# Kernel tuning notes

Hardware: AMD Instinct MI355X
Metric: run time of the kernel (lower is better)

## Reference

```python
import jax, jax.numpy as jnp
import numpy as np

EMBED_DIM = 384
HEADS = 6
HEAD_DIM = EMBED_DIM // HEADS
WINDOW = 64


def setup_inputs() -> dict:
    key = jax.random.key(0)
    ks = jax.random.split(key, 5)
    B, T = 128, 256
    s_attn = 1.0 / np.sqrt(EMBED_DIM)
    x = jax.random.normal(ks[0], (B, T, EMBED_DIM), dtype=jnp.float32)
    W_attn = jax.random.normal(ks[1], (EMBED_DIM, 3 * EMBED_DIM), dtype=jnp.float32) * s_attn
    b_attn = jax.random.normal(ks[2], (3 * EMBED_DIM,), dtype=jnp.float32) * 0.02
    W_proj = jax.random.normal(ks[3], (EMBED_DIM, EMBED_DIM), dtype=jnp.float32) * s_attn
    b_proj = jax.random.normal(ks[4], (EMBED_DIM,), dtype=jnp.float32) * 0.02
    return {"x": x, "W_attn": W_attn, "b_attn": b_attn, "W_proj": W_proj, "b_proj": b_proj}


def reference(x, W_attn, b_attn, W_proj, b_proj):
    B, T, C = x.shape
    qkv = x @ W_attn + b_attn  # [B,T,3C]
    q, k, v = jnp.split(qkv, 3, axis=-1)
    # [B, H, T, hd]
    q = q.reshape(B, T, HEADS, HEAD_DIM).transpose(0, 2, 1, 3)
    k = k.reshape(B, T, HEADS, HEAD_DIM).transpose(0, 2, 1, 3)
    v = v.reshape(B, T, HEADS, HEAD_DIM).transpose(0, 2, 1, 3)
    scale = 1.0 / np.sqrt(HEAD_DIM).astype(np.float32)
    att = jnp.einsum('bhqd,bhkd->bhqk', q, k) * scale
    i = jnp.arange(T)
    causal = i[:, None] >= i[None, :]
    local = jnp.abs(i[:, None] - i[None, :]) <= WINDOW
    mask = (causal & local)[None, None, :, :]
    att = jnp.where(mask, att, -jnp.inf)
    att = jax.nn.softmax(att, axis=-1)
    y = jnp.einsum('bhqk,bhkd->bhqd', att, v)
    y = y.transpose(0, 2, 1, 3).reshape(B, T, C)
    return y @ W_proj + b_proj
```

## Files before the change

kernel.cpp:

```cpp
#include <hip/hip_runtime.h>

#define B_SZ   128
#define T_SEQ  256
#define C_DIM  384
#define HEADS  6
#define HD     64
#define WIN    64

typedef __bf16 bf16x8 __attribute__((ext_vector_type(8)));
typedef float  f32x4  __attribute__((ext_vector_type(4)));

typedef __attribute__((address_space(3))) void lds_void;
typedef __attribute__((address_space(1))) void gbl_void;

__device__ __forceinline__ unsigned short f2bf(float f) {
  unsigned u = __float_as_uint(f);
  u += 0x7FFFu + ((u >> 16) & 1u);
  return (unsigned short)(u >> 16);
}

__global__ __launch_bounds__(256) void convert_f32_bf16(
    const float* __restrict__ in, unsigned short* __restrict__ out, int n4) {
  int i = blockIdx.x * blockDim.x + threadIdx.x;
  if (i < n4) {
    float4 v = ((const float4*)in)[i];
    ushort4 o;
    o.x = f2bf(v.x); o.y = f2bf(v.y); o.z = f2bf(v.z); o.w = f2bf(v.w);
    ((ushort4*)out)[i] = o;
  }
}

__global__ __launch_bounds__(256) void transpose_convert(
    const float* __restrict__ in, unsigned short* __restrict__ out,
    int K, int N) {
  __shared__ float tile[32][33];
  const int gx = blockIdx.x * 32;
  const int gy = blockIdx.y * 32;
  const int tx = threadIdx.x;
  const int ty = threadIdx.y;
#pragma unroll
  for (int r = ty; r < 32; r += 8)
    tile[r][tx] = in[(size_t)(gy + r) * N + gx + tx];
  __syncthreads();
#pragma unroll
  for (int r = ty; r < 32; r += 8)
    out[(size_t)(gx + r) * K + gy + tx] = f2bf(tile[tx][r]);
}

template <bool OUT_BF16>
__global__ __launch_bounds__(256) void gemm_mfma_bf16(
    const unsigned short* __restrict__ A,
    const unsigned short* __restrict__ Bt,
    const float* __restrict__ bias,
    void* __restrict__ Cv, int M, int N, int K) {
  __shared__ unsigned short As[128 * 64];
  __shared__ unsigned short Bs[128 * 64];

  const int t    = threadIdx.x;
  const int lane = t & 63;
  const int w    = t >> 6;
  const int wm   = w & 1;
  const int wn   = w >> 1;
  const int m0   = blockIdx.y * 128;
  const int n0   = blockIdx.x * 128;

  const int lrow = lane >> 3;
  const int lcol = lane & 7;
  const int schunk = lcol ^ lrow;

  f32x4 acc[4][4];
#pragma unroll
  for (int i = 0; i < 4; ++i)
#pragma unroll
    for (int j = 0; j < 4; ++j) acc[i][j] = (f32x4){0.f, 0.f, 0.f, 0.f};

  const int mfrag = lane & 15;
  const int quad  = lane >> 4;
  const int sw    = mfrag & 7;

  for (int k0 = 0; k0 < K; k0 += 64) {
#pragma unroll
    for (int i = 0; i < 4; ++i) {
      const int inst = w * 4 + i;
      const int r = inst * 8 + lrow;
      const unsigned short* ga = A  + (size_t)(m0 + r) * K + k0 + schunk * 8;
      const unsigned short* gb = Bt + (size_t)(n0 + r) * K + k0 + schunk * 8;
      __builtin_amdgcn_global_load_lds((const gbl_void*)ga,
                                       (lds_void*)(As + inst * 512), 16, 0, 0);
      __builtin_amdgcn_global_load_lds((const gbl_void*)gb,
                                       (lds_void*)(Bs + inst * 512), 16, 0, 0);
    }
    __syncthreads();

#pragma unroll
    for (int ks = 0; ks < 64; ks += 32) {
      const int cg = (ks >> 3) + quad;
      const int cp = (cg ^ sw) << 3;
      bf16x8 af[4], bfr[4];
#pragma unroll
      for (int mt = 0; mt < 4; ++mt)
        af[mt] = *(const bf16x8*)(As + (size_t)(wm * 64 + mt * 16 + mfrag) * 64 + cp);
#pragma unroll
      for (int nt = 0; nt < 4; ++nt)
        bfr[nt] = *(const bf16x8*)(Bs + (size_t)(wn * 64 + nt * 16 + mfrag) * 64 + cp);
#pragma unroll
      for (int mt = 0; mt < 4; ++mt)
#pragma unroll
        for (int nt = 0; nt < 4; ++nt)
          acc[mt][nt] = __builtin_amdgcn_mfma_f32_16x16x32_bf16(
              af[mt], bfr[nt], acc[mt][nt], 0, 0, 0);
    }
    __syncthreads();
  }

  const int ccol = lane & 15;
  const int crow = (lane >> 4) * 4;
#pragma unroll
  for (int nt = 0; nt < 4; ++nt) {
    const int col = n0 + wn * 64 + nt * 16 + ccol;
    const float bv = bias[col];
#pragma unroll
    for (int mt = 0; mt < 4; ++mt) {
#pragma unroll
      for (int r = 0; r < 4; ++r) {
        const int row = m0 + wm * 64 + mt * 16 + crow + r;
        const float val = acc[mt][nt][r] + bv;
        if (OUT_BF16)
          ((unsigned short*)Cv)[(size_t)row * N + col] = f2bf(val);
        else
          ((float*)Cv)[(size_t)row * N + col] = val;
      }
    }
  }
}

#define PSTR 68
__global__ __launch_bounds__(256) void attn_mfma(
    const unsigned short* __restrict__ qkv, unsigned short* __restrict__ y) {
  __shared__ unsigned short Qs[64 * 64];
  __shared__ unsigned short Ks[64 * 64];
  __shared__ unsigned short Vt[64 * 64];
  __shared__ float Pw[4][16 * PSTR];

  const int bid = blockIdx.x;
  const int qt  = bid & 3;
  const int h   = (bid >> 2) % HEADS;
  const int b   = bid / (4 * HEADS);
  const int t   = threadIdx.x;
  const int lane = t & 63;
  const int w    = t >> 6;
  const int quad = lane >> 4;
  const int m16  = lane & 15;
  const int sw   = m16 & 7;

  const size_t rowbase = (size_t)b * T_SEQ * (3 * C_DIM);
  const int qoff = h * HD;
  const int koff = C_DIM + h * HD;
  const int voff = 2 * C_DIM + h * HD;
  const int qg0  = qt * 64;

  const int lrow = lane >> 3;
  const int lcol = lane & 7;
  const int schunk = lcol ^ lrow;

#pragma unroll
  for (int i = 0; i < 2; ++i) {
    const int inst = w * 2 + i;
    const int r = inst * 8 + lrow;
    const unsigned short* ga =
        qkv + rowbase + (size_t)(qg0 + r) * (3 * C_DIM) + qoff + schunk * 8;
    __builtin_amdgcn_global_load_lds((const gbl_void*)ga,
                                     (lds_void*)(Qs + inst * 512), 16, 0, 0);
  }

  float m_r[4], l_r[4];
  f32x4 yacc[4];
#pragma unroll
  for (int r = 0; r < 4; ++r) { m_r[r] = -1e30f; l_r[r] = 0.f; }
#pragma unroll
  for (int dt = 0; dt < 4; ++dt) yacc[dt] = (f32x4){0.f, 0.f, 0.f, 0.f};

  const int nchunks  = (qt == 0) ? 1 : 2;
  const int kb_first = (qt == 0) ? 0 : (qg0 - 64);
  const int qrow_base = qg0 + w * 16 + quad * 4;

  for (int ch = 0; ch < nchunks; ++ch) {
    const int kb = kb_first + ch * 64;

    __syncthreads();

#pragma unroll
    for (int i = 0; i < 2; ++i) {
      const int inst = w * 2 + i;
      const int r = inst * 8 + lrow;
      const unsigned short* ga =
          qkv + rowbase + (size_t)(kb + r) * (3 * C_DIM) + koff + schunk * 8;
      __builtin_amdgcn_global_load_lds((const gbl_void*)ga,
                                       (lds_void*)(Ks + inst * 512), 16, 0, 0);
    }
    {
      const int vkey = t & 63;
      const int kc = vkey >> 3, ke = vkey & 7;
      const int vd0  = (t >> 6) * 16;
      const unsigned short* gv =
          qkv + rowbase + (size_t)(kb + vkey) * (3 * C_DIM) + voff + vd0;
#pragma unroll
      for (int u = 0; u < 4; ++u) {
        ushort4 vv = *(const ushort4*)(gv + u * 4);
#pragma unroll
        for (int jj = 0; jj < 4; ++jj) {
          const int d = vd0 + u * 4 + jj;
          const unsigned short val =
              (jj == 0) ? vv.x : (jj == 1) ? vv.y : (jj == 2) ? vv.z : vv.w;
          Vt[d * 64 + ((kc ^ (d & 7)) << 3) + ke] = val;
        }
      }
    }
    __syncthreads();

    f32x4 sacc[4];
#pragma unroll
    for (int nt = 0; nt < 4; ++nt) sacc[nt] = (f32x4){0.f, 0.f, 0.f, 0.f};
#pragma unroll
    for (int ks = 0; ks < 64; ks += 32) {
      const int cp = (((ks >> 3) + quad) ^ sw) << 3;
      bf16x8 aq = *(const bf16x8*)(Qs + (size_t)(w * 16 + m16) * 64 + cp);
#pragma unroll
      for (int nt = 0; nt < 4; ++nt) {
        bf16x8 kf = *(const bf16x8*)(Ks + (size_t)(nt * 16 + m16) * 64 + cp);
        sacc[nt] = __builtin_amdgcn_mfma_f32_16x16x32_bf16(aq, kf, sacc[nt], 0, 0, 0);
      }
    }

    float mc[4] = {-1e30f, -1e30f, -1e30f, -1e30f};
#pragma unroll
    for (int nt = 0; nt < 4; ++nt) {
      const int kg = kb + nt * 16 + m16;
#pragma unroll
      for (int r = 0; r < 4; ++r) {
        const int qg = qrow_base + r;
        const bool valid = (kg <= qg) && (qg - kg <= WIN);
        const float sv = valid ? (sacc[nt][r] * 0.125f) : -1e30f;
        sacc[nt][r] = sv;
        mc[r] = fmaxf(mc[r], sv);
      }
    }
#pragma unroll
    for (int r = 0; r < 4; ++r) {
#pragma unroll
      for (int x = 1; x <= 8; x <<= 1) mc[r] = fmaxf(mc[r], __shfl_xor(mc[r], x));
    }

#pragma unroll
    for (int r = 0; r < 4; ++r) {
      const float mn    = fmaxf(m_r[r], mc[r]);
      const float alpha = __expf(m_r[r] - mn);
      m_r[r] = mn;
      l_r[r] *= alpha;
#pragma unroll
      for (int dt = 0; dt < 4; ++dt) yacc[dt][r] *= alpha;
      float ls = 0.f;
#pragma unroll
      for (int nt = 0; nt < 4; ++nt) {
        const float p = __expf(sacc[nt][r] - mn);
        sacc[nt][r] = p;
        ls += p;
      }
#pragma unroll
      for (int x = 1; x <= 8; x <<= 1) ls += __shfl_xor(ls, x);
      l_r[r] += ls;
    }

#pragma unroll
    for (int nt = 0; nt < 4; ++nt)
#pragma unroll
      for (int r = 0; r < 4; ++r)
        Pw[w][(quad * 4 + r) * PSTR + nt * 16 + m16] = sacc[nt][r];
    __syncthreads();

#pragma unroll
    for (int ks = 0; ks < 64; ks += 32) {
      f32x4 pa = *(const f32x4*)(&Pw[w][m16 * PSTR + ks + quad * 8]);
      f32x4 pb = *(const f32x4*)(&Pw[w][m16 * PSTR + ks + quad * 8 + 4]);
      bf16x8 ap;
#pragma unroll
      for (int j = 0; j < 4; ++j) {
        ap[j]     = (__bf16)pa[j];
        ap[4 + j] = (__bf16)pb[j];
      }
      const int cp = (((ks >> 3) + quad) ^ sw) << 3;
#pragma unroll
      for (int dt = 0; dt < 4; ++dt) {
        bf16x8 vf = *(const bf16x8*)(Vt + (size_t)(dt * 16 + m16) * 64 + cp);
        yacc[dt] = __builtin_amdgcn_mfma_f32_16x16x32_bf16(ap, vf, yacc[dt], 0, 0, 0);
      }
    }
  }

  float inv[4];
#pragma unroll
  for (int r = 0; r < 4; ++r) inv[r] = 1.f / l_r[r];
#pragma unroll
  for (int dt = 0; dt < 4; ++dt) {
#pragma unroll
    for (int r = 0; r < 4; ++r) {
      const int row = qrow_base + r;
      y[((size_t)(b * T_SEQ + row)) * C_DIM + h * HD + dt * 16 + m16] =
          f2bf(yacc[dt][r] * inv[r]);
    }
  }
}

extern "C" void kernel_launch(void* const* d_in, const int* in_sizes, int n_in,
                              void* d_out, int out_size, void* d_ws, size_t ws_size,
                              hipStream_t stream) {
  const float* x      = (const float*)d_in[0];
  const float* W_attn = (const float*)d_in[1];
  const float* b_attn = (const float*)d_in[2];
  const float* W_proj = (const float*)d_in[3];
  const float* b_proj = (const float*)d_in[4];
  float* out = (float*)d_out;

  const int M = B_SZ * T_SEQ;

  unsigned short* qkv_b = (unsigned short*)d_ws;
  unsigned short* y_b   = qkv_b + (size_t)M * (3 * C_DIM);
  unsigned short* x_b   = y_b   + (size_t)M * C_DIM;
  unsigned short* Wa_t  = x_b   + (size_t)M * C_DIM;
  unsigned short* Wp_t  = Wa_t  + (size_t)(3 * C_DIM) * C_DIM;

  {
    int n4 = M * C_DIM / 4;
    convert_f32_bf16<<<n4 / 256, 256, 0, stream>>>(x, x_b, n4);
    transpose_convert<<<dim3((3 * C_DIM) / 32, C_DIM / 32), dim3(32, 8), 0, stream>>>(
        W_attn, Wa_t, C_DIM, 3 * C_DIM);
    transpose_convert<<<dim3(C_DIM / 32, C_DIM / 32), dim3(32, 8), 0, stream>>>(
        W_proj, Wp_t, C_DIM, C_DIM);
  }

  gemm_mfma_bf16<true><<<dim3((3 * C_DIM) / 128, M / 128), 256, 0, stream>>>(
      x_b, Wa_t, b_attn, qkv_b, M, 3 * C_DIM, C_DIM);

  attn_mfma<<<dim3(B_SZ * HEADS * (T_SEQ / 64)), 256, 0, stream>>>(qkv_b, y_b);

  gemm_mfma_bf16<false><<<dim3(C_DIM / 128, M / 128), 256, 0, stream>>>(
      y_b, Wp_t, b_proj, out, M, C_DIM, C_DIM);
}
```

Before: 224.7 us.

## Stage GEMM/attention epilogues through LDS for vector stores and remap blocks per XCD

The GEMM and attention epilogues now write accumulators into shared memory, then issue coalesced 4-wide vector stores to global memory instead of scattered scalar writes. Block indices are permuted so consecutive logical tiles land on the same XCD, improving L2 locality for shared A rows and K/V data. The GEMM launch becomes 1D with an explicit tiles_n parameter. This adds extra LDS traffic and synchronisation in the epilogue, and the remap assumes grid sizes divisible by 8.

```diff
diff --git a/kernel.cpp b/kernel.cpp
--- a/kernel.cpp
+++ b/kernel.cpp
@@ -52,17 +52,24 @@
     const unsigned short* __restrict__ A,
     const unsigned short* __restrict__ Bt,
     const float* __restrict__ bias,
-    void* __restrict__ Cv, int M, int N, int K) {
-  __shared__ unsigned short As[128 * 64];
-  __shared__ unsigned short Bs[128 * 64];
+    void* __restrict__ Cv, int M, int N, int K, int tiles_n) {
+  __shared__ __attribute__((aligned(16))) char smem_raw[64 * 132 * 4];
+  unsigned short* As = (unsigned short*)smem_raw;
+  unsigned short* Bs = As + 128 * 64;
+  float* ep = (float*)smem_raw;
 
   const int t    = threadIdx.x;
   const int lane = t & 63;
   const int w    = t >> 6;
   const int wm   = w & 1;
   const int wn   = w >> 1;
-  const int m0   = blockIdx.y * 128;
-  const int n0   = blockIdx.x * 128;
+
+  const unsigned id    = blockIdx.x;
+  const unsigned remap = (id & 7u) * (gridDim.x >> 3) + (id >> 3);
+  const int by = remap / (unsigned)tiles_n;
+  const int bx = remap % (unsigned)tiles_n;
+  const int m0 = by * 128;
+  const int n0 = bx * 128;
 
   const int lrow = lane >> 3;
   const int lcol = lane & 7;
@@ -94,8 +101,7 @@
 
 #pragma unroll
     for (int ks = 0; ks < 64; ks += 32) {
-      const int cg = (ks >> 3) + quad;
-      const int cp = (cg ^ sw) << 3;
+      const int cp = (((ks >> 3) + quad) ^ sw) << 3;
       bf16x8 af[4], bfr[4];
 #pragma unroll
       for (int mt = 0; mt < 4; ++mt)
@@ -113,22 +119,38 @@
     __syncthreads();
   }
 
-  const int ccol = lane & 15;
-  const int crow = (lane >> 4) * 4;
-#pragma unroll
-  for (int nt = 0; nt < 4; ++nt) {
-    const int col = n0 + wn * 64 + nt * 16 + ccol;
-    const float bv = bias[col];
-#pragma unroll
-    for (int mt = 0; mt < 4; ++mt) {
-#pragma unroll
-      for (int r = 0; r < 4; ++r) {
-        const int row = m0 + wm * 64 + mt * 16 + crow + r;
-        const float val = acc[mt][nt][r] + bv;
-        if (OUT_BF16)
-          ((unsigned short*)Cv)[(size_t)row * N + col] = f2bf(val);
-        else
-          ((float*)Cv)[(size_t)row * N + col] = val;
+  float bv[4];
+#pragma unroll
+  for (int nt = 0; nt < 4; ++nt) bv[nt] = bias[n0 + wn * 64 + nt * 16 + mfrag];
+
+#pragma unroll
+  for (int p = 0; p < 2; ++p) {
+    if (p) __syncthreads();
+    if (wm == p) {
+#pragma unroll
+      for (int mt = 0; mt < 4; ++mt)
+#pragma unroll
+        for (int nt = 0; nt < 4; ++nt)
+#pragma unroll
+          for (int r = 0; r < 4; ++r)
+            ep[(mt * 16 + quad * 4 + r) * 132 + wn * 64 + nt * 16 + mfrag] =
+                acc[mt][nt][r] + bv[nt];
+    }
+    __syncthreads();
+#pragma unroll
+    for (int cc = 0; cc < 8; ++cc) {
+      const int chunk = cc * 256 + t;
+      const int row = chunk >> 5;
+      const int c4  = chunk & 31;
+      f32x4 v = *(const f32x4*)(ep + row * 132 + c4 * 4);
+      const int grow = m0 + p * 64 + row;
+      const int gcol = n0 + c4 * 4;
+      if (OUT_BF16) {
+        ushort4 o;
+        o.x = f2bf(v[0]); o.y = f2bf(v[1]); o.z = f2bf(v[2]); o.w = f2bf(v[3]);
+        *(ushort4*)((unsigned short*)Cv + (size_t)grow * N + gcol) = o;
+      } else {
+        *(f32x4*)((float*)Cv + (size_t)grow * N + gcol) = v;
       }
     }
   }
@@ -142,7 +164,8 @@
   __shared__ unsigned short Vt[64 * 64];
   __shared__ float Pw[4][16 * PSTR];
 
-  const int bid = blockIdx.x;
+  const unsigned id  = blockIdx.x;
+  const unsigned bid = (id & 7u) * (gridDim.x >> 3) + (id >> 3);
   const int qt  = bid & 3;
   const int h   = (bid >> 2) % HEADS;
   const int b   = bid / (4 * HEADS);
@@ -297,17 +320,25 @@
     }
   }
 
+  float* epy = &Pw[0][0];
   float inv[4];
 #pragma unroll
   for (int r = 0; r < 4; ++r) inv[r] = 1.f / l_r[r];
 #pragma unroll
-  for (int dt = 0; dt < 4; ++dt) {
-#pragma unroll
-    for (int r = 0; r < 4; ++r) {
-      const int row = qrow_base + r;
-      y[((size_t)(b * T_SEQ + row)) * C_DIM + h * HD + dt * 16 + m16] =
-          f2bf(yacc[dt][r] * inv[r]);
-    }
+  for (int dt = 0; dt < 4; ++dt)
+#pragma unroll
+    for (int r = 0; r < 4; ++r)
+      epy[(w * 16 + quad * 4 + r) * PSTR + dt * 16 + m16] = yacc[dt][r] * inv[r];
+  __syncthreads();
+#pragma unroll
+  for (int cc = 0; cc < 4; ++cc) {
+    const int chunk = cc * 256 + t;
+    const int row = chunk >> 4;
+    const int c4  = chunk & 15;
+    f32x4 v = *(const f32x4*)(epy + row * PSTR + c4 * 4);
+    ushort4 o;
+    o.x = f2bf(v[0]); o.y = f2bf(v[1]); o.z = f2bf(v[2]); o.w = f2bf(v[3]);
+    *(ushort4*)(y + (size_t)(b * T_SEQ + qg0 + row) * C_DIM + h * HD + c4 * 4) = o;
   }
 }
 
@@ -338,11 +369,11 @@
         W_proj, Wp_t, C_DIM, C_DIM);
   }
 
-  gemm_mfma_bf16<true><<<dim3((3 * C_DIM) / 128, M / 128), 256, 0, stream>>>(
-      x_b, Wa_t, b_attn, qkv_b, M, 3 * C_DIM, C_DIM);
+  gemm_mfma_bf16<true><<<dim3(9 * (M / 128)), 256, 0, stream>>>(
+      x_b, Wa_t, b_attn, qkv_b, M, 3 * C_DIM, C_DIM, 9);
 
   attn_mfma<<<dim3(B_SZ * HEADS * (T_SEQ / 64)), 256, 0, stream>>>(qkv_b, y_b);
 
-  gemm_mfma_bf16<false><<<dim3(C_DIM / 128, M / 128), 256, 0, stream>>>(
-      y_b, Wp_t, b_proj, out, M, C_DIM, C_DIM);
-}
+  gemm_mfma_bf16<false><<<dim3(3 * (M / 128)), 256, 0, stream>>>(
+      y_b, Wp_t, b_proj, out, M, C_DIM, C_DIM, 3);
+}
```

Result: faster. 211.9 us (-5.7%).
